# Kernel tuning notes

Hardware: AMD Instinct MI355X
Metric: run time of the kernel (lower is better)

## Reference

```python
import jax, jax.numpy as jnp
import numpy as np

NUM_HEADS = 12
EPSILON = 1e-6
SCORE_SCALE = 1.0


def setup_inputs() -> dict:
    key = jax.random.key(0)
    ks = jax.random.split(key, 5)
    B, L, E = 2, 2048, 768
    x = jax.random.normal(ks[0], (B, L, E), dtype=jnp.float32)
    attention_mask = jnp.ones((B, L), dtype=jnp.int32)
    # linear params (lecun-ish scale)
    Wqkv = jax.random.normal(ks[1], (E, 3 * E), dtype=jnp.float32) / np.sqrt(E)
    bqkv = jnp.zeros((3 * E,), dtype=jnp.float32)
    Wout = jax.random.normal(ks[2], (E, E), dtype=jnp.float32) / np.sqrt(E)
    bout = jnp.zeros((E,), dtype=jnp.float32)
    return {"x": x, "attention_mask": attention_mask, "Wqkv": Wqkv,
            "bqkv": bqkv, "Wout": Wout, "bout": bout}


def reference(x, attention_mask, Wqkv, bqkv, Wout, bout):
    B, L, E = x.shape
    H = NUM_HEADS
    D = E // H
    qkv = x @ Wqkv + bqkv                      # [B,L,3E]
    q, k, v = jnp.split(qkv, 3, axis=-1)
    q = q.reshape(B, L, H, D).transpose(0, 2, 1, 3)  # [B,H,L,D]
    k = k.reshape(B, L, H, D).transpose(0, 2, 1, 3)
    v = v.reshape(B, L, H, D).transpose(0, 2, 1, 3)

    dot = jnp.einsum('bhid,bhjd->bhij', q, k)        # [B,H,L,L]
    q_sq = jnp.sum(q * q, axis=-1)[..., :, None]     # [B,H,L,1]
    k_sq = jnp.sum(k * k, axis=-1)[..., None, :]     # [B,H,1,L]
    scores = (dot * dot) / (q_sq + k_sq - 2.0 * dot + EPSILON)
    scores = scores * SCORE_SCALE

    pad = attention_mask[:, None, None, :]           # [B,1,1,L]
    scores = jnp.where(pad == 1, scores, jnp.finfo(scores.dtype).min)

    attn = jax.nn.softmax(scores, axis=-1)
    out = jnp.einsum('bhij,bhjd->bhid', attn, v)     # [B,H,L,D]
    out = out.transpose(0, 2, 1, 3).reshape(B, L, E)
    return out @ Wout + bout
```

## Files before the change

kernel.cpp:

```cpp
#include <hip/hip_runtime.h>
#include <hip/hip_bf16.h>
#include <cstdint>
#include <cstddef>


typedef __bf16 bf16_t;
typedef __bf16 bf16x8 __attribute__((ext_vector_type(8)));
typedef __bf16 bf16x4 __attribute__((ext_vector_type(4)));
typedef float floatx4 __attribute__((ext_vector_type(4)));

#define DEVI static __device__ __forceinline__

#define Bc 2
#define Lc 2048
#define Ec 768
#define Hc 12
#define Dc 64
#define N3c 2304
#define Mc 4096
#define ROWSc (Bc * Hc * Lc)

DEVI void glds16(const bf16_t* g, bf16_t* l) {
  __builtin_amdgcn_global_load_lds(
      (const __attribute__((address_space(1))) void*)g,
      (__attribute__((address_space(3))) void*)l, 16, 0, 0);
}

__global__ __launch_bounds__(256) void k_prep(
    const float* __restrict__ x, bf16_t* __restrict__ xb,
    const float* __restrict__ Wqkv, bf16_t* __restrict__ WqT,
    const float* __restrict__ Wout, bf16_t* __restrict__ WoT) {
  __shared__ float tile[32][33];
  const int bid = blockIdx.x, tid = threadIdx.x;
  if (bid < 3072) {
    const int i = (bid * 256 + tid) * 4;
    float4 v = *(const float4*)(x + i);
    bf16x4 o;
    o[0] = (bf16_t)v.x; o[1] = (bf16_t)v.y; o[2] = (bf16_t)v.z; o[3] = (bf16_t)v.w;
    *(bf16x4*)(xb + i) = o;
    return;
  }
  const float* in; bf16_t* out; int C, local;
  if (bid < 4800) { local = bid - 3072; in = Wqkv; out = WqT; C = N3c; }
  else            { local = bid - 4800; in = Wout; out = WoT; C = Ec;  }
  const int R = Ec;
  const int nbx = C / 32;
  const int c0 = (local % nbx) * 32, r0 = (local / nbx) * 32;
  const int tx = tid & 31, ty = tid >> 5;
  #pragma unroll
  for (int i = 0; i < 32; i += 8)
    tile[ty + i][tx] = in[(size_t)(r0 + ty + i) * C + c0 + tx];
  __syncthreads();
  #pragma unroll
  for (int i = 0; i < 32; i += 8)
    out[(size_t)(c0 + ty + i) * R + r0 + tx] = (bf16_t)tile[tx][ty + i];
}


DEVI void gemm_core(const bf16_t* __restrict__ A, const bf16_t* __restrict__ Bt,
                    bf16_t* lA, bf16_t* lB, int m0, int n0, floatx4 (&acc)[4][4]) {
  const int tid = threadIdx.x, wave = tid >> 6, lane = tid & 63;
  const int wm = (wave >> 1) * 64, wn = (wave & 1) * 64;
  const int lrow = lane >> 2, lseg = lane & 3;
  const int quad = lane >> 4, r16 = lane & 15;
  for (int kk = 0; kk < 768; kk += 32) {
    glds16(A  + (size_t)(m0 + wave * 32      + lrow) * 768 + kk + lseg * 8, lA + (wave * 32) * 32);
    glds16(A  + (size_t)(m0 + wave * 32 + 16 + lrow) * 768 + kk + lseg * 8, lA + (wave * 32 + 16) * 32);
    glds16(Bt + (size_t)(n0 + wave * 32      + lrow) * 768 + kk + lseg * 8, lB + (wave * 32) * 32);
    glds16(Bt + (size_t)(n0 + wave * 32 + 16 + lrow) * 768 + kk + lseg * 8, lB + (wave * 32 + 16) * 32);
    __syncthreads();
    bf16x8 af[4], bv[4];
    #pragma unroll
    for (int mi = 0; mi < 4; mi++)
      af[mi] = *(const bf16x8*)(lA + (wm + mi * 16 + r16) * 32 + quad * 8);
    #pragma unroll
    for (int ni = 0; ni < 4; ni++)
      bv[ni] = *(const bf16x8*)(lB + (wn + ni * 16 + r16) * 32 + quad * 8);
    #pragma unroll
    for (int mi = 0; mi < 4; mi++)
      #pragma unroll
      for (int ni = 0; ni < 4; ni++)
        acc[mi][ni] = __builtin_amdgcn_mfma_f32_16x16x32_bf16(af[mi], bv[ni], acc[mi][ni], 0, 0, 0);
    __syncthreads();
  }
}

__global__ __launch_bounds__(256) void k_gemm_qkv(
    const bf16_t* __restrict__ A, const bf16_t* __restrict__ Bt,
    const float* __restrict__ bias,
    bf16_t* __restrict__ Qo, bf16_t* __restrict__ Ko, bf16_t* __restrict__ VTo) {
  __shared__ bf16_t lA[128 * 32];
  __shared__ bf16_t lB[128 * 32];
  const int m0 = blockIdx.y * 128, n0 = blockIdx.x * 128;
  const int tid = threadIdx.x, wave = tid >> 6, lane = tid & 63;
  const int wm = (wave >> 1) * 64, wn = (wave & 1) * 64;
  const int quad = lane >> 4, r16 = lane & 15;
  floatx4 acc[4][4] = {};
  gemm_core(A, Bt, lA, lB, m0, n0, acc);

  const int sec = n0 / 768;
  if (sec < 2) {
    bf16_t* dst = (sec == 0) ? Qo : Ko;
    #pragma unroll
    for (int ni = 0; ni < 4; ni++) {
      const int n = n0 + wn + ni * 16 + r16;
      const int nn = n - sec * 768;
      const int h = nn >> 6, d = nn & 63;
      const float bvs = bias[n];
      #pragma unroll
      for (int mi = 0; mi < 4; mi++) {
        #pragma unroll
        for (int reg = 0; reg < 4; reg++) {
          const int m = m0 + wm + mi * 16 + quad * 4 + reg;
          const int b = m >> 11, l = m & 2047;
          const float v = acc[mi][ni][reg] + bvs;
          dst[(((size_t)(b * Hc + h)) * Lc + l) * Dc + d] = (bf16_t)v;
        }
      }
    }
  } else {
    #pragma unroll
    for (int ni = 0; ni < 4; ni++) {
      const int n = n0 + wn + ni * 16 + r16;
      const int nn = n - 1536;
      const int h = nn >> 6, d = nn & 63;
      const float bvs = bias[n];
      #pragma unroll
      for (int mi = 0; mi < 4; mi++) {
        const int m = m0 + wm + mi * 16 + quad * 4;
        const int b = m >> 11, l = m & 2047;
        bf16x4 o;
        #pragma unroll
        for (int reg = 0; reg < 4; reg++)
          o[reg] = (bf16_t)(acc[mi][ni][reg] + bvs);
        *(bf16x4*)(VTo + (((size_t)(b * Hc + h)) * Dc + d) * Lc + l) = o;
      }
    }
  }
}

__global__ __launch_bounds__(256) void k_gemm_out(
    const bf16_t* __restrict__ A, const bf16_t* __restrict__ Bt,
    const float* __restrict__ bias, float* __restrict__ out) {
  __shared__ bf16_t lA[128 * 32];
  __shared__ bf16_t lB[128 * 32];
  const int m0 = blockIdx.y * 128, n0 = blockIdx.x * 128;
  const int tid = threadIdx.x, wave = tid >> 6, lane = tid & 63;
  const int wm = (wave >> 1) * 64, wn = (wave & 1) * 64;
  const int quad = lane >> 4, r16 = lane & 15;
  floatx4 acc[4][4] = {};
  gemm_core(A, Bt, lA, lB, m0, n0, acc);
  #pragma unroll
  for (int ni = 0; ni < 4; ni++) {
    const int n = n0 + wn + ni * 16 + r16;
    const float bvs = bias[n];
    #pragma unroll
    for (int mi = 0; mi < 4; mi++) {
      #pragma unroll
      for (int reg = 0; reg < 4; reg++) {
        const int m = m0 + wm + mi * 16 + quad * 4 + reg;
        out[(size_t)m * Ec + n] = acc[mi][ni][reg] + bvs;
      }
    }
  }
}

__global__ __launch_bounds__(256) void k_prep2(
    const bf16_t* __restrict__ Q, const bf16_t* __restrict__ K,
    const int* __restrict__ mask,
    float* __restrict__ qsq, float* __restrict__ ksq,
    float* __restrict__ mbias) {
  const int row = blockIdx.x * 256 + threadIdx.x;
  const bf16x8* q = (const bf16x8*)(Q + (size_t)row * 64);
  const bf16x8* k = (const bf16x8*)(K + (size_t)row * 64);
  float sq = 0.f, sk = 0.f;
  #pragma unroll
  for (int c = 0; c < 8; c++) {
    bf16x8 vq = q[c], vk = k[c];
    #pragma unroll
    for (int j = 0; j < 8; j++) {
      float a = (float)vq[j]; sq += a * a;
      float b = (float)vk[j]; sk += b * b;
    }
  }
  qsq[row] = sq;
  ksq[row] = sk + 1e-6f;
  const int bh = row >> 11, l = row & 2047;
  if (bh == 0 || bh == Hc) {
    const int b = bh / Hc;
    mbias[b * Lc + l] = (mask[b * Lc + l] == 1) ? 0.f : -1e30f;
  }
}

__global__ __launch_bounds__(256) void k_attn(
    const bf16_t* __restrict__ Q, const bf16_t* __restrict__ K,
    const bf16_t* __restrict__ VT, const float* __restrict__ qsq,
    const float* __restrict__ ksq, const float* __restrict__ mbias,
    bf16_t* __restrict__ AO) {
  __shared__ bf16_t lK[2][4096];
  __shared__ bf16_t lV[2][4096];
  __shared__ bf16_t lP[4][16 * 64];
  const int gid0 = blockIdx.x;
  const int gid = (gid0 & 7) * 96 + (gid0 >> 3);
  const int bh = gid >> 5, qt = gid & 31;
  const int b = bh / Hc;
  const int h = bh - b * Hc;
  const int tid = threadIdx.x, wave = tid >> 6, lane = tid & 63;
  const int quad = lane >> 4, r16 = lane & 15;
  const int q0 = qt * 64 + wave * 16;
  const bf16_t* Qh = Q + ((size_t)bh * Lc) * Dc;
  const bf16_t* Kh = K + ((size_t)bh * Lc) * Dc;
  const bf16_t* VTh = VT + ((size_t)bh * Dc) * Lc;
  const float* qsqh = qsq + bh * Lc;
  const float* ksqh = ksq + bh * Lc;
  const float* mbb = mbias + b * Lc;
  bf16_t* myP = &lP[wave][0];

  const int p0 = wave * 64 + lane;
  const int srow = p0 >> 3;
  const int sj = (p0 & 7) ^ (srow & 7);
  const bf16_t* kg0 = Kh + (size_t)srow * 64 + sj * 8;
  const bf16_t* kg1 = kg0 + 32 * 64;
  const bf16_t* vg0 = VTh + (size_t)srow * Lc + sj * 8;
  const bf16_t* vg1 = vg0 + 32 * Lc;
  const int ld0 = wave * 64 * 8, ld1 = (256 + wave * 64) * 8;

  const int sl0 = ((quad ^ (r16 & 7)) * 8);
  const int sl1 = sl0 ^ 32;
  const int pswz = r16 & 7;

  bf16x8 qf0 = *(const bf16x8*)(Qh + (size_t)(q0 + r16) * 64 + quad * 8);
  bf16x8 qf1 = *(const bf16x8*)(Qh + (size_t)(q0 + r16) * 64 + 32 + quad * 8);
  const float qs = qsqh[q0 + r16];
  float mi = -1e30f;
  float li = 0.f;
  floatx4 of[4] = {};

  glds16(kg0, &lK[0][ld0]);
  glds16(kg1, &lK[0][ld1]);
  glds16(vg0, &lV[0][ld0]);
  glds16(vg1, &lV[0][ld1]);
  kg0 += 4096; kg1 += 4096; vg0 += 64; vg1 += 64;
  float4 ks4[4], mb4[4];
  #pragma unroll
  for (int c = 0; c < 4; c++) {
    float4 kv = *(const float4*)(ksqh + c * 16 + quad * 4);
    ks4[c] = make_float4(kv.x + qs, kv.y + qs, kv.z + qs, kv.w + qs);
    mb4[c] = *(const float4*)(mbb + c * 16 + quad * 4);
  }
  __syncthreads();

  const int nt = Lc / 64;
  for (int t = 0; t < nt; t++) {
    const int cur = t & 1;
    const bool more = (t + 1 < nt);
    if (more) {
      const int nxt = cur ^ 1;
      glds16(kg0, &lK[nxt][ld0]);
      glds16(kg1, &lK[nxt][ld1]);
      glds16(vg0, &lV[nxt][ld0]);
      glds16(vg1, &lV[nxt][ld1]);
      kg0 += 4096; kg1 += 4096; vg0 += 64; vg1 += 64;
    }
    float4 ks4n[4], mb4n[4];
    if (more) {
      const int ktn = (t + 1) * 64;
      #pragma unroll
      for (int c = 0; c < 4; c++) {
        ks4n[c] = *(const float4*)(ksqh + ktn + c * 16 + quad * 4);
        mb4n[c] = *(const float4*)(mbb + ktn + c * 16 + quad * 4);
      }
    }
    floatx4 dot[4];
    __builtin_amdgcn_s_setprio(1);
    #pragma unroll
    for (int c = 0; c < 4; c++) {
      const int rbase = (c * 16 + r16) * 64;
      bf16x8 kf0 = *(const bf16x8*)(&lK[cur][rbase + sl0]);
      bf16x8 kf1 = *(const bf16x8*)(&lK[cur][rbase + sl1]);
      floatx4 a = {};
      a = __builtin_amdgcn_mfma_f32_16x16x32_bf16(kf0, qf0, a, 0, 0, 0);
      a = __builtin_amdgcn_mfma_f32_16x16x32_bf16(kf1, qf1, a, 0, 0, 0);
      dot[c] = a;
    }
    __builtin_amdgcn_s_setprio(0);
    float rmax = -1e30f;
    #pragma unroll
    for (int c = 0; c < 4; c++) {
      #pragma unroll
      for (int reg = 0; reg < 4; reg++) {
        const float dd = dot[c][reg];
        const float qks = ((const float*)&ks4[c])[reg];
        const float mbv = ((const float*)&mb4[c])[reg];
        const float den = __builtin_fmaf(dd, -2.f, qks);
        const float sc = __builtin_fmaf((dd * 1.44269504f) * dd,
                                        __builtin_amdgcn_rcpf(den), mbv);
        dot[c][reg] = sc;
        rmax = fmaxf(rmax, sc);
      }
    }
    if (!__all(rmax <= mi + 11.5416f)) {
      float rg = fmaxf(rmax, __shfl_xor(rmax, 16));
      rg = fmaxf(rg, __shfl_xor(rg, 32));
      const float mnew = fmaxf(mi, rg);
      const float alpha = exp2f(mi - mnew);
      li *= alpha;
      #pragma unroll
      for (int t4 = 0; t4 < 4; t4++) {
        #pragma unroll
        for (int reg = 0; reg < 4; reg++) of[t4][reg] *= alpha;
      }
      mi = mnew;
    }
    float psum = 0.f;
    #pragma unroll
    for (int c = 0; c < 4; c++) {
      bf16x4 pk;
      #pragma unroll
      for (int reg = 0; reg < 4; reg++) {
        const float p = exp2f(dot[c][reg] - mi);
        psum += p;
        pk[reg] = (bf16_t)p;
      }
      const int jw = (2 * c + (quad >> 1)) ^ pswz;
      *(bf16x4*)(myP + r16 * 64 + jw * 8 + (quad & 1) * 4) = pk;
    }
    li += psum;
    bf16x8 pf0 = *(const bf16x8*)(myP + r16 * 64 + (quad ^ pswz) * 8);
    bf16x8 pf1 = *(const bf16x8*)(myP + r16 * 64 + ((4 + quad) ^ pswz) * 8);
    __builtin_amdgcn_s_setprio(1);
    #pragma unroll
    for (int t4 = 0; t4 < 4; t4++) {
      const int rbase = (t4 * 16 + r16) * 64;
      bf16x8 vf0 = *(const bf16x8*)(&lV[cur][rbase + sl0]);
      bf16x8 vf1 = *(const bf16x8*)(&lV[cur][rbase + sl1]);
      of[t4] = __builtin_amdgcn_mfma_f32_16x16x32_bf16(vf0, pf0, of[t4], 0, 0, 0);
      of[t4] = __builtin_amdgcn_mfma_f32_16x16x32_bf16(vf1, pf1, of[t4], 0, 0, 0);
    }
    __builtin_amdgcn_s_setprio(0);
    if (more) {
      #pragma unroll
      for (int c = 0; c < 4; c++) {
        ks4[c] = make_float4(ks4n[c].x + qs, ks4n[c].y + qs,
                             ks4n[c].z + qs, ks4n[c].w + qs);
        mb4[c] = mb4n[c];
      }
    }
    __syncthreads();
  }
  li += __shfl_xor(li, 16);
  li += __shfl_xor(li, 32);
  const float inv = (li > 0.f) ? __builtin_amdgcn_rcpf(li) : 0.f;
  bf16_t* aor = AO + ((size_t)(b * Lc + q0 + r16)) * Ec + h * 64;
  #pragma unroll
  for (int t4 = 0; t4 < 4; t4++) {
    bf16x4 o;
    #pragma unroll
    for (int reg = 0; reg < 4; reg++) o[reg] = (bf16_t)(of[t4][reg] * inv);
    *(bf16x4*)(aor + t4 * 16 + quad * 4) = o;
  }
}


extern "C" void kernel_launch(void* const* d_in, const int* in_sizes, int n_in,
                              void* d_out, int out_size, void* d_ws, size_t ws_size,
                              hipStream_t stream) {
  const float* x    = (const float*)d_in[0];
  const int*   mask = (const int*)d_in[1];
  const float* Wqkv = (const float*)d_in[2];
  const float* bqkv = (const float*)d_in[3];
  const float* Wout = (const float*)d_in[4];
  const float* bout = (const float*)d_in[5];
  float* out = (float*)d_out;

  auto al = [](size_t x) { return (x + 255) & ~(size_t)255; };
  char* ws = (char*)d_ws;
  size_t off = 0;
  auto carve = [&](size_t bytes) -> char* {
    char* p = ws + off;
    off += al(bytes);
    return p;
  };
  bf16_t* WoT = (bf16_t*)carve((size_t)Ec * Ec * 2);
  bf16_t* Qb  = (bf16_t*)carve((size_t)ROWSc * Dc * 2);
  bf16_t* Kb  = (bf16_t*)carve((size_t)ROWSc * Dc * 2);
  bf16_t* VTb = (bf16_t*)carve((size_t)ROWSc * Dc * 2);
  bf16_t* AOb = (bf16_t*)carve((size_t)Mc * Ec * 2);
  float*  qsq = (float*)carve((size_t)ROWSc * 4);
  float*  ksq = (float*)carve((size_t)ROWSc * 4);
  float*  mbias = (float*)carve((size_t)Bc * Lc * 4);
  const size_t uni = off;
  bf16_t* xb  = (bf16_t*)(ws + uni);
  bf16_t* WqT = (bf16_t*)(ws + uni + al((size_t)Mc * Ec * 2));
  (void)in_sizes; (void)n_in; (void)out_size; (void)ws_size;

  k_prep<<<5376, 256, 0, stream>>>(x, xb, Wqkv, WqT, Wout, WoT);
  k_gemm_qkv<<<dim3(N3c / 128, Mc / 128), 256, 0, stream>>>(xb, WqT, bqkv, Qb, Kb, VTb);
  k_prep2<<<192, 256, 0, stream>>>(Qb, Kb, mask, qsq, ksq, mbias);
  k_attn<<<dim3(ROWSc / 64), 256, 0, stream>>>(Qb, Kb, VTb, qsq, ksq, mbias, AOb);
  k_gemm_out<<<dim3(Ec / 128, Mc / 128), 256, 0, stream>>>(AOb, WoT, bout, out);
}
```

Measured before the change: 211.4 us.

## Fuse norm and mask prep into GEMM epilogue and prep; double-buffer GEMM LDS

The separate k_prep2 kernel is removed. The squared norms of Q and K rows are now computed in the QKV GEMM epilogue, using a lane shuffle reduction across the 16 columns of each head. The mask bias is computed in extra blocks of k_prep. The shared GEMM core also now double-buffers its LDS tiles, so the next K-slice is prefetched while MFMAs run on the current one. This removes a kernel launch and a reread of Q/K, and hides load latency, at the cost of twice the LDS per GEMM block and a heavier epilogue.

```diff
diff --git a/kernel.cpp b/kernel.cpp
--- a/kernel.cpp
+++ b/kernel.cpp
@@ -29,7 +29,8 @@
 __global__ __launch_bounds__(256) void k_prep(
     const float* __restrict__ x, bf16_t* __restrict__ xb,
     const float* __restrict__ Wqkv, bf16_t* __restrict__ WqT,
-    const float* __restrict__ Wout, bf16_t* __restrict__ WoT) {
+    const float* __restrict__ Wout, bf16_t* __restrict__ WoT,
+    const int* __restrict__ mask, float* __restrict__ mbias) {
   __shared__ float tile[32][33];
   const int bid = blockIdx.x, tid = threadIdx.x;
   if (bid < 3072) {
@@ -38,6 +39,11 @@
     bf16x4 o;
     o[0] = (bf16_t)v.x; o[1] = (bf16_t)v.y; o[2] = (bf16_t)v.z; o[3] = (bf16_t)v.w;
     *(bf16x4*)(xb + i) = o;
+    return;
+  }
+  if (bid >= 5376) {
+    const int i = (bid - 5376) * 256 + tid;
+    mbias[i] = (mask[i] == 1) ? 0.f : -1e30f;
     return;
   }
   const float* in; bf16_t* out; int C, local;
@@ -56,26 +62,36 @@
     out[(size_t)(c0 + ty + i) * R + r0 + tx] = (bf16_t)tile[tx][ty + i];
 }
 
-
 DEVI void gemm_core(const bf16_t* __restrict__ A, const bf16_t* __restrict__ Bt,
                     bf16_t* lA, bf16_t* lB, int m0, int n0, floatx4 (&acc)[4][4]) {
   const int tid = threadIdx.x, wave = tid >> 6, lane = tid & 63;
   const int wm = (wave >> 1) * 64, wn = (wave & 1) * 64;
   const int lrow = lane >> 2, lseg = lane & 3;
   const int quad = lane >> 4, r16 = lane & 15;
+  const bf16_t* a0 = A + (size_t)(m0 + wave * 32 + lrow) * 768 + lseg * 8;
+  const bf16_t* a1 = A + (size_t)(m0 + wave * 32 + 16 + lrow) * 768 + lseg * 8;
+  const bf16_t* b0 = Bt + (size_t)(n0 + wave * 32 + lrow) * 768 + lseg * 8;
+  const bf16_t* b1 = Bt + (size_t)(n0 + wave * 32 + 16 + lrow) * 768 + lseg * 8;
+  const int la0 = (wave * 32) * 32, la1 = (wave * 32 + 16) * 32;
+  glds16(a0, lA + la0); glds16(a1, lA + la1);
+  glds16(b0, lB + la0); glds16(b1, lB + la1);
+  __syncthreads();
   for (int kk = 0; kk < 768; kk += 32) {
-    glds16(A  + (size_t)(m0 + wave * 32      + lrow) * 768 + kk + lseg * 8, lA + (wave * 32) * 32);
-    glds16(A  + (size_t)(m0 + wave * 32 + 16 + lrow) * 768 + kk + lseg * 8, lA + (wave * 32 + 16) * 32);
-    glds16(Bt + (size_t)(n0 + wave * 32      + lrow) * 768 + kk + lseg * 8, lB + (wave * 32) * 32);
-    glds16(Bt + (size_t)(n0 + wave * 32 + 16 + lrow) * 768 + kk + lseg * 8, lB + (wave * 32 + 16) * 32);
-    __syncthreads();
+    const int cur = (kk >> 5) & 1;
+    if (kk + 32 < 768) {
+      const int nb = (cur ^ 1) * 4096;
+      glds16(a0 + kk + 32, lA + nb + la0); glds16(a1 + kk + 32, lA + nb + la1);
+      glds16(b0 + kk + 32, lB + nb + la0); glds16(b1 + kk + 32, lB + nb + la1);
+    }
+    const bf16_t* lac = lA + cur * 4096;
+    const bf16_t* lbc = lB + cur * 4096;
     bf16x8 af[4], bv[4];
     #pragma unroll
     for (int mi = 0; mi < 4; mi++)
-      af[mi] = *(const bf16x8*)(lA + (wm + mi * 16 + r16) * 32 + quad * 8);
+      af[mi] = *(const bf16x8*)(lac + (wm + mi * 16 + r16) * 32 + quad * 8);
     #pragma unroll
     for (int ni = 0; ni < 4; ni++)
-      bv[ni] = *(const bf16x8*)(lB + (wn + ni * 16 + r16) * 32 + quad * 8);
+      bv[ni] = *(const bf16x8*)(lbc + (wn + ni * 16 + r16) * 32 + quad * 8);
     #pragma unroll
     for (int mi = 0; mi < 4; mi++)
       #pragma unroll
@@ -88,9 +104,10 @@
 __global__ __launch_bounds__(256) void k_gemm_qkv(
     const bf16_t* __restrict__ A, const bf16_t* __restrict__ Bt,
     const float* __restrict__ bias,
-    bf16_t* __restrict__ Qo, bf16_t* __restrict__ Ko, bf16_t* __restrict__ VTo) {
-  __shared__ bf16_t lA[128 * 32];
-  __shared__ bf16_t lB[128 * 32];
+    bf16_t* __restrict__ Qo, bf16_t* __restrict__ Ko, bf16_t* __restrict__ VTo,
+    float* __restrict__ qsq, float* __restrict__ ksq) {
+  __shared__ bf16_t lA[2 * 128 * 32];
+  __shared__ bf16_t lB[2 * 128 * 32];
   const int m0 = blockIdx.y * 128, n0 = blockIdx.x * 128;
   const int tid = threadIdx.x, wave = tid >> 6, lane = tid & 63;
   const int wm = (wave >> 1) * 64, wn = (wave & 1) * 64;
@@ -101,11 +118,18 @@
   const int sec = n0 / 768;
   if (sec < 2) {
     bf16_t* dst = (sec == 0) ? Qo : Ko;
+    float* sqo = (sec == 0) ? qsq : ksq;
+    const float epsadd = (sec == 0) ? 0.f : 1e-6f;
+    const int h = ((n0 + wn) - sec * 768) >> 6;
+    float part[4][4];
+    #pragma unroll
+    for (int mi = 0; mi < 4; mi++)
+      #pragma unroll
+      for (int reg = 0; reg < 4; reg++) part[mi][reg] = 0.f;
     #pragma unroll
     for (int ni = 0; ni < 4; ni++) {
       const int n = n0 + wn + ni * 16 + r16;
-      const int nn = n - sec * 768;
-      const int h = nn >> 6, d = nn & 63;
+      const int d = (n - sec * 768) & 63;
       const float bvs = bias[n];
       #pragma unroll
       for (int mi = 0; mi < 4; mi++) {
@@ -113,8 +137,26 @@
         for (int reg = 0; reg < 4; reg++) {
           const int m = m0 + wm + mi * 16 + quad * 4 + reg;
           const int b = m >> 11, l = m & 2047;
-          const float v = acc[mi][ni][reg] + bvs;
-          dst[(((size_t)(b * Hc + h)) * Lc + l) * Dc + d] = (bf16_t)v;
+          const bf16_t v = (bf16_t)(acc[mi][ni][reg] + bvs);
+          dst[(((size_t)(b * Hc + h)) * Lc + l) * Dc + d] = v;
+          const float vr = (float)v;
+          part[mi][reg] += vr * vr;
+        }
+      }
+    }
+    #pragma unroll
+    for (int mi = 0; mi < 4; mi++) {
+      #pragma unroll
+      for (int reg = 0; reg < 4; reg++) {
+        float s = part[mi][reg];
+        s += __shfl_xor(s, 1);
+        s += __shfl_xor(s, 2);
+        s += __shfl_xor(s, 4);
+        s += __shfl_xor(s, 8);
+        if (r16 == 0) {
+          const int m = m0 + wm + mi * 16 + quad * 4 + reg;
+          const int b = m >> 11, l = m & 2047;
+          sqo[(size_t)(b * Hc + h) * Lc + l] = s + epsadd;
         }
       }
     }
@@ -142,8 +184,8 @@
 __global__ __launch_bounds__(256) void k_gemm_out(
     const bf16_t* __restrict__ A, const bf16_t* __restrict__ Bt,
     const float* __restrict__ bias, float* __restrict__ out) {
-  __shared__ bf16_t lA[128 * 32];
-  __shared__ bf16_t lB[128 * 32];
+  __shared__ bf16_t lA[2 * 128 * 32];
+  __shared__ bf16_t lB[2 * 128 * 32];
   const int m0 = blockIdx.y * 128, n0 = blockIdx.x * 128;
   const int tid = threadIdx.x, wave = tid >> 6, lane = tid & 63;
   const int wm = (wave >> 1) * 64, wn = (wave & 1) * 64;
@@ -162,33 +204,6 @@
         out[(size_t)m * Ec + n] = acc[mi][ni][reg] + bvs;
       }
     }
-  }
-}
-
-__global__ __launch_bounds__(256) void k_prep2(
-    const bf16_t* __restrict__ Q, const bf16_t* __restrict__ K,
-    const int* __restrict__ mask,
-    float* __restrict__ qsq, float* __restrict__ ksq,
-    float* __restrict__ mbias) {
-  const int row = blockIdx.x * 256 + threadIdx.x;
-  const bf16x8* q = (const bf16x8*)(Q + (size_t)row * 64);
-  const bf16x8* k = (const bf16x8*)(K + (size_t)row * 64);
-  float sq = 0.f, sk = 0.f;
-  #pragma unroll
-  for (int c = 0; c < 8; c++) {
-    bf16x8 vq = q[c], vk = k[c];
-    #pragma unroll
-    for (int j = 0; j < 8; j++) {
-      float a = (float)vq[j]; sq += a * a;
-      float b = (float)vk[j]; sk += b * b;
-    }
-  }
-  qsq[row] = sq;
-  ksq[row] = sk + 1e-6f;
-  const int bh = row >> 11, l = row & 2047;
-  if (bh == 0 || bh == Hc) {
-    const int b = bh / Hc;
-    mbias[b * Lc + l] = (mask[b * Lc + l] == 1) ? 0.f : -1e30f;
   }
 }
 
@@ -394,9 +409,8 @@
   bf16_t* WqT = (bf16_t*)(ws + uni + al((size_t)Mc * Ec * 2));
   (void)in_sizes; (void)n_in; (void)out_size; (void)ws_size;
 
-  k_prep<<<5376, 256, 0, stream>>>(x, xb, Wqkv, WqT, Wout, WoT);
-  k_gemm_qkv<<<dim3(N3c / 128, Mc / 128), 256, 0, stream>>>(xb, WqT, bqkv, Qb, Kb, VTb);
-  k_prep2<<<192, 256, 0, stream>>>(Qb, Kb, mask, qsq, ksq, mbias);
+  k_prep<<<5392, 256, 0, stream>>>(x, xb, Wqkv, WqT, Wout, WoT, mask, mbias);
+  k_gemm_qkv<<<dim3(N3c / 128, Mc / 128), 256, 0, stream>>>(xb, WqT, bqkv, Qb, Kb, VTb, qsq, ksq);
   k_attn<<<dim3(ROWSc / 64), 256, 0, stream>>>(Qb, Kb, VTb, qsq, ksq, mbias, AOb);
   k_gemm_out<<<dim3(Ec / 128, Mc / 128), 256, 0, stream>>>(AOb, WoT, bout, out);
 }
```

After: 220.2 us. 4.2% more time.
